# Optimization experiments

Measured on AMD Instinct MI355X. Metric: run time of the kernel, lower is better.

Reference implementation:

```python
import jax, jax.numpy as jnp
import numpy as np

DIM = 512
BATCH = 256
LOG_2PI = float(np.log(2.0 * np.pi))


def setup_inputs() -> dict:
    key = jax.random.key(0)
    k_x, k_mu, k_ld, k_lt, k_m = jax.random.split(key, 5)
    n_tril = DIM * (DIM - 1) // 2  # 130816
    x = jax.random.normal(k_x, (BATCH, DIM), dtype=jnp.float32)
    mu = jax.random.normal(k_mu, (DIM,), dtype=jnp.float32)
    log_diagonal = jax.random.normal(k_ld, (DIM,), dtype=jnp.float32)
    # scale strict-lower entries for reasonable conditioning of cov = A A^T
    lower_tri = jax.random.normal(k_lt, (n_tril,), dtype=jnp.float32) * 0.05
    mask = jax.random.randint(k_m, (BATCH, DIM), 0, 2) > 0
    return {"x": x, "mu": mu, "log_diagonal": log_diagonal,
            "lower_tri": lower_tri, "mask": mask}


def _build_cov(log_diagonal, lower_tri):
    D = log_diagonal.shape[0]
    ti, tj = np.tril_indices(D, -1)
    A = jnp.zeros((D, D), dtype=log_diagonal.dtype).at[ti, tj].set(lower_tri)
    A = A + jnp.diag(jnp.exp(log_diagonal))
    return A @ A.T  # SPD covariance [D, D]


def reference(x, mu, log_diagonal, lower_tri, mask):
    cov = _build_cov(log_diagonal, lower_tri)          # [D, D]
    m = mask.astype(x.dtype)                           # [B, D]
    D = cov.shape[0]
    # Block-diagonalized masked covariance: observed block = cov[m][:,m],
    # unobserved block = identity. Equivalent to per-sample submatrix gather.
    cov_m = (m[:, :, None] * m[:, None, :]) * cov[None] \
            + jnp.eye(D, dtype=x.dtype)[None] * (1.0 - m)[:, :, None]  # [B, D, D]
    L = jnp.linalg.cholesky(cov_m)                     # batched [B, D, D]
    r = (x - mu) * m                                   # masked residual [B, D]
    z = jax.scipy.linalg.solve_triangular(L, r[..., None], lower=True)[..., 0]
    quad = jnp.sum(z * z, axis=-1)                     # [B]
    # unobserved diag of L is 1 -> contributes 0 to logdet
    logdet = 2.0 * jnp.sum(jnp.log(jnp.diagonal(L, axis1=-2, axis2=-1)), axis=-1)
    d_obs = jnp.sum(m, axis=-1)
    return 0.5 * (quad + logdet + d_obs * LOG_2PI)     # neg log prob, [B]
```

## Files before the change

kernel.cpp:

```cpp
#include <hip/hip_runtime.h>
#include <hip/hip_bf16.h>

#define LOG_2PI 1.8378770664093453f
#define R0 256
#define GSTRIDE 512
#define TRI_FLOATS 33280
#define CSTR 68
#define NT 256
#define SMEM_FLOATS (TRI_FLOATS + 512 + 512 + 512 + 16 + 64*CSTR)
#define SMEM_BYTES (SMEM_FLOATS * 4)

__device__ __forceinline__ int tribase(int r) {
    int m = r & 3;
    return r * (r + 1) / 2 + 6 * (r >> 2) + ((m * (7 - m)) >> 1);
}

__global__ __launch_bounds__(256) void build_A(const float* __restrict__ logd,
                                               const float* __restrict__ lt,
                                               float* __restrict__ A) {
    int idx = blockIdx.x * 256 + threadIdx.x;
    int i = idx >> 9, j = idx & 511;
    float v;
    if (j < i)       v = lt[(i * (i - 1)) / 2 + j];
    else if (j == i) v = expf(logd[i]);
    else             v = 0.f;
    A[idx] = v;
}

__global__ __launch_bounds__(256) void aat(const float* __restrict__ A,
                                           float* __restrict__ C) {
    __shared__ float Ash[32][33];
    __shared__ float Bsh[32][33];
    int tx = threadIdx.x & 31, ty = threadIdx.x >> 5;
    int bi = blockIdx.y, bj = blockIdx.x;
    float acc[4] = {0.f, 0.f, 0.f, 0.f};
    for (int k0 = 0; k0 < 512; k0 += 32) {
        #pragma unroll
        for (int q = 0; q < 4; q++) {
            int r = ty + q * 8;
            Ash[r][tx] = A[(bi * 32 + r) * 512 + k0 + tx];
            Bsh[r][tx] = A[(bj * 32 + r) * 512 + k0 + tx];
        }
        __syncthreads();
        for (int c = 0; c < 32; c++) {
            float bv = Bsh[tx][c];
            #pragma unroll
            for (int q = 0; q < 4; q++) acc[q] += Ash[ty + q * 8][c] * bv;
        }
        __syncthreads();
    }
    #pragma unroll
    for (int q = 0; q < 4; q++)
        C[(bi * 32 + ty + q * 8) * 512 + bj * 32 + tx] = acc[q];
}

__global__ __launch_bounds__(256) void compact(const float* __restrict__ x,
                                               const float* __restrict__ mu,
                                               const int* __restrict__ mask,
                                               int* __restrict__ obs_idx,
                                               int* __restrict__ n_obs,
                                               float* __restrict__ rc) {
    int b = blockIdx.x, t = threadIdx.x;
    __shared__ int wsum[4];
    int i0 = 2 * t, i1 = 2 * t + 1;
    int m0 = (mask[b * 512 + i0] != 0) ? 1 : 0;
    int m1 = (mask[b * 512 + i1] != 0) ? 1 : 0;
    int local = m0 + m1;
    int v = local;
    int lane = t & 63, wv = t >> 6;
    #pragma unroll
    for (int off = 1; off < 64; off <<= 1) {
        int u = __shfl_up(v, off, 64);
        if (lane >= off) v += u;
    }
    if (lane == 63) wsum[wv] = v;
    __syncthreads();
    int woff = 0;
    for (int w = 0; w < wv; w++) woff += wsum[w];
    int excl = woff + v - local;
    if (m0) { obs_idx[b * 512 + excl] = i0; rc[b * 512 + excl] = x[b * 512 + i0] - mu[i0]; }
    if (m1) { int p = excl + m0; obs_idx[b * 512 + p] = i1; rc[b * 512 + p] = x[b * 512 + i1] - mu[i1]; }
    if (t == 0) n_obs[b] = wsum[0] + wsum[1] + wsum[2] + wsum[3];
}

template <typename RPF>
__device__ __forceinline__ void diag_block(RPF rptr, float* zsh, float* dinvAll,
                                           float& llog, int j0, int nb, int n, int tid) {
    if (tid < 32) {
        int l = tid;
        int r = j0 + l;
        float a[32];
        float z = 0.f;
        if (r < n) {
            const float4* src = (const float4*)(rptr(r) + j0);
            #pragma unroll
            for (int q = 0; q < 8; q++) {
                float4 t = src[q];
                a[4*q+0] = t.x; a[4*q+1] = t.y; a[4*q+2] = t.z; a[4*q+3] = t.w;
            }
            z = zsh[r];
        } else {
            #pragma unroll
            for (int q = 0; q < 32; q++) a[q] = 0.f;
        }
        float dv = 0.f;
        #pragma unroll
        for (int k = 0; k < 32; k++) {
            if (k < nb) {
                float akk = __shfl(a[k], k, 64);
                float rin = rsqrtf(akk);
                float lkk = akk * rin;
                if (l == k) { dv = rin; llog += __logf(lkk); }
                a[k] = (l == k) ? lkk : a[k] * rin;
                #pragma unroll
                for (int j = k + 1; j < 32; j++) {
                    float ajk = __shfl(a[k], j, 64);
                    a[j] -= a[k] * ajk;
                }
            }
        }
        #pragma unroll
        for (int k = 0; k < 32; k++) {
            if (k < nb) {
                if (l == k) z *= dv;
                float zk = __shfl(z, k, 64);
                if (l > k) z -= a[k] * zk;
            }
        }
        dinvAll[j0 + l] = dv;
        if (l < nb) {
            zsh[r] = z;
            float* dst = rptr(r) + j0;
            #pragma unroll
            for (int c = 0; c < 32; c++)
                if (c <= l) dst[c] = a[c];
        }
    }
}

__global__ __launch_bounds__(NT) void chol_solve(
    const float* __restrict__ cov, const float* __restrict__ rc,
    const int* __restrict__ obs_idx, const int* __restrict__ n_obs,
    float* __restrict__ gtail_all, float* __restrict__ out) {

    extern __shared__ float smem[];
    float* T       = smem;
    float* zsh     = T + TRI_FLOATS;
    int*   oi      = (int*)(zsh + 512);
    float* dinvAll = (float*)(oi + 512);
    float* red     = dinvAll + 512;
    float* SBc     = red + 16;

    int b = blockIdx.x, tid = threadIdx.x;
    int lane = tid & 63, wv = tid >> 6;
    int n = n_obs[b]; if (n > 512) n = 512;
    float* gtail = gtail_all + (size_t)b * 256 * GSTRIDE;
    if (n == 0) { if (tid == 0) out[b] = 0.f; return; }

    for (int i = tid; i < n; i += NT) {
        oi[i] = obs_idx[b * 512 + i];
        zsh[i] = rc[b * 512 + i];
    }
    __syncthreads();

    int n0 = (n < R0) ? n : R0;
    int ntail = n - n0;

    for (int r = wv; r < n0; r += 4) {
        const float* crow = cov + (size_t)oi[r] * 512;
        float* dst = T + tribase(r);
        #pragma unroll 4
        for (int j = lane; j <= r; j += 64) dst[j] = crow[oi[j]];
    }
    for (int r = n0 + wv; r < n; r += 4) {
        const float* crow = cov + (size_t)oi[r] * 512;
        float* dst = gtail + (size_t)(r - n0) * GSTRIDE;
        #pragma unroll 4
        for (int j = lane; j < n0; j += 64) dst[j] = crow[oi[j]];
    }
    __syncthreads();

    float llog = 0.f;

    for (int j0 = 0; j0 < n0; j0 += 32) {
        int nb = min(32, n0 - j0);
        diag_block([&](int r) { return T + tribase(r); },
                   zsh, dinvAll, llog, j0, nb, n0, tid);
        __syncthreads();

        int mL = n0 - j0 - 32; if (mL < 0) mL = 0;
        int mtot = mL + ntail;
        if (mtot > 0) {
            for (int idx = tid; idx < mtot; idx += NT) {
                int r; float* prow;
                if (idx < mL) { r = j0 + 32 + idx; prow = T + tribase(r) + j0; }
                else          { r = n0 + (idx - mL);
                                prow = gtail + (size_t)(idx - mL) * GSTRIDE + j0; }
                float p[32];
                #pragma unroll
                for (int q = 0; q < 8; q++) {
                    float4 t = *(const float4*)&prow[4 * q];
                    p[4*q+0] = t.x; p[4*q+1] = t.y; p[4*q+2] = t.z; p[4*q+3] = t.w;
                }
                #pragma unroll
                for (int j = 0; j < 32; j++) {
                    float acc = p[j];
                    const float* dj = T + tribase(j0 + j) + j0;
                    int jf = j >> 2;
                    for (int q2 = 0; q2 < jf; q2++) {
                        float4 t = *(const float4*)&dj[q2 * 4];
                        acc -= p[q2*4+0]*t.x + p[q2*4+1]*t.y + p[q2*4+2]*t.z + p[q2*4+3]*t.w;
                    }
                    for (int c = jf * 4; c < j; c++) acc -= p[c] * dj[c];
                    p[j] = acc * dinvAll[j0 + j];
                }
                float zu = 0.f;
                #pragma unroll
                for (int q = 0; q < 8; q++) {
                    *(float4*)&prow[4 * q] = make_float4(p[4*q], p[4*q+1], p[4*q+2], p[4*q+3]);
                    float4 zz = *(const float4*)&zsh[j0 + 4 * q];
                    zu += p[4*q]*zz.x + p[4*q+1]*zz.y + p[4*q+2]*zz.z + p[4*q+3]*zz.w;
                }
                zsh[r] -= zu;
            }
            __syncthreads();

            if (mL > 0) {
                int nMac = (mL + 63) >> 6;
                int ty = tid >> 4, tx = tid & 15;
                for (int MI = 0; MI < nMac; MI++)
                    for (int MJ = 0; MJ <= MI; MJ++) {
                        int rbase = j0 + 32 + MI * 64 + ty * 4;
                        int cbase = j0 + 32 + MJ * 64 + tx * 4;
                        if (MI == MJ && cbase > rbase + 3) continue;
                        int ra[4], rb[4];
                        #pragma unroll
                        for (int a = 0; a < 4; a++) {
                            ra[a] = tribase(min(rbase + a, n0 - 1)) + j0;
                            rb[a] = tribase(min(cbase + a, n0 - 1)) + j0;
                        }
                        float acc[4][4];
                        #pragma unroll
                        for (int a = 0; a < 4; a++)
                            #pragma unroll
                            for (int c = 0; c < 4; c++) acc[a][c] = 0.f;
                        #pragma unroll
                        for (int q = 0; q < 8; q++) {
                            float4 av[4], bv[4];
                            #pragma unroll
                            for (int a = 0; a < 4; a++) av[a] = *(const float4*)&T[ra[a] + 4 * q];
                            #pragma unroll
                            for (int c = 0; c < 4; c++) bv[c] = *(const float4*)&T[rb[c] + 4 * q];
                            #pragma unroll
                            for (int a = 0; a < 4; a++)
                                #pragma unroll
                                for (int c = 0; c < 4; c++)
                                    acc[a][c] += av[a].x*bv[c].x + av[a].y*bv[c].y +
                                                 av[a].z*bv[c].z + av[a].w*bv[c].w;
                        }
                        #pragma unroll
                        for (int a = 0; a < 4; a++) {
                            int r = rbase + a;
                            if (r < n0) {
                                float* trow = T + tribase(r);
                                if (cbase + 3 <= r) {
                                    float4 v = *(const float4*)&trow[cbase];
                                    v.x -= acc[a][0]; v.y -= acc[a][1];
                                    v.z -= acc[a][2]; v.w -= acc[a][3];
                                    *(float4*)&trow[cbase] = v;
                                } else {
                                    #pragma unroll
                                    for (int c = 0; c < 4; c++) {
                                        int cl = cbase + c;
                                        if (cl <= r) trow[cl] -= acc[a][c];
                                    }
                                }
                            }
                        }
                    }
            }

            if (ntail > 0 && mL > 0) {
                int nch = mL >> 2;
                int ntask = ntail * nch;
                for (int t = tid; t < ntask; t += NT) {
                    int row = t / nch, ch = t % nch;
                    float* grow = gtail + (size_t)row * GSTRIDE;
                    float w[32];
                    #pragma unroll
                    for (int q = 0; q < 8; q++) {
                        float4 t4 = *(const float4*)&grow[j0 + 4 * q];
                        w[4*q+0] = t4.x; w[4*q+1] = t4.y; w[4*q+2] = t4.z; w[4*q+3] = t4.w;
                    }
                    int jb = j0 + 32 + ch * 4;
                    float acc4[4];
                    #pragma unroll
                    for (int c = 0; c < 4; c++) {
                        const float* dj = T + tribase(jb + c) + j0;
                        float s = 0.f;
                        #pragma unroll
                        for (int q = 0; q < 8; q++) {
                            float4 t4 = *(const float4*)&dj[4 * q];
                            s += w[4*q+0]*t4.x + w[4*q+1]*t4.y + w[4*q+2]*t4.z + w[4*q+3]*t4.w;
                        }
                        acc4[c] = s;
                    }
                    float4 g4 = *(const float4*)&grow[jb];
                    g4.x -= acc4[0]; g4.y -= acc4[1]; g4.z -= acc4[2]; g4.w -= acc4[3];
                    *(float4*)&grow[jb] = g4;
                }
            }
            __syncthreads();
        }
    }

    for (int gs2 = R0; gs2 < n; gs2 += 64) {
        int t1 = min(64, n - gs2);
        int g1 = gs2 - R0;

        for (int cp = R0; cp < gs2; cp += 32) {
            if (tid < t1) {
                int r = gs2 + tid;
                float* row = gtail + (size_t)(r - R0) * GSTRIDE;
                const float* crow = cov + (size_t)oi[r] * 512;
                float zacc = 0.f;
                for (int j = 0; j < 32; j++) {
                    int jj = cp + j;
                    const float* Lrow = gtail + (size_t)(jj - R0) * GSTRIDE;
                    float acc = crow[oi[jj]];
                    for (int c = 0; c < jj; c++) acc -= row[c] * Lrow[c];
                    float wv2 = acc * dinvAll[jj];
                    row[jj] = wv2;
                    zacc += wv2 * zsh[jj];
                }
                zsh[r] -= zacc;
            }
            __syncthreads();
        }

        {
            int npair = t1 * (t1 + 1) / 2;
            for (int e = tid; e < npair; e += NT) {
                int ti = (int)((sqrtf(8.f * (float)e + 1.f) - 1.f) * 0.5f);
                while ((ti + 1) * (ti + 2) / 2 <= e) ti++;
                while (ti * (ti + 1) / 2 > e) ti--;
                int tj = e - ti * (ti + 1) / 2;
                const float* wa = gtail + (size_t)(g1 + ti) * GSTRIDE;
                const float* wb = gtail + (size_t)(g1 + tj) * GSTRIDE;
                float s = 0.f;
                for (int k = 0; k < gs2; k += 4) {
                    float4 a4 = *(const float4*)&wa[k];
                    float4 b4 = *(const float4*)&wb[k];
                    s += a4.x*b4.x + a4.y*b4.y + a4.z*b4.z + a4.w*b4.w;
                }
                SBc[ti * CSTR + tj] = cov[(size_t)oi[gs2 + ti] * 512 + oi[gs2 + tj]] - s;
            }
        }
        __syncthreads();

        auto crptr = [&](int r) { return SBc + (r - gs2) * CSTR - gs2; };
        diag_block(crptr, zsh, dinvAll, llog, gs2, min(32, t1), n, tid);
        __syncthreads();
        if (t1 > 32) {
            int t2 = t1 - 32;
            if (tid < t2) {
                int r = gs2 + 32 + tid;
                float* prow = SBc + (32 + tid) * CSTR;
                float p[32];
                #pragma unroll
                for (int q = 0; q < 8; q++) {
                    float4 t = *(const float4*)&prow[4 * q];
                    p[4*q+0] = t.x; p[4*q+1] = t.y; p[4*q+2] = t.z; p[4*q+3] = t.w;
                }
                #pragma unroll
                for (int j = 0; j < 32; j++) {
                    float acc = p[j];
                    const float* dj = SBc + j * CSTR;
                    for (int c = 0; c < j; c++) acc -= p[c] * dj[c];
                    p[j] = acc * dinvAll[gs2 + j];
                }
                float zu = 0.f;
                #pragma unroll
                for (int q = 0; q < 8; q++) {
                    *(float4*)&prow[4 * q] = make_float4(p[4*q], p[4*q+1], p[4*q+2], p[4*q+3]);
                    float4 zz = *(const float4*)&zsh[gs2 + 4 * q];
                    zu += p[4*q]*zz.x + p[4*q+1]*zz.y + p[4*q+2]*zz.z + p[4*q+3]*zz.w;
                }
                zsh[r] -= zu;
            }
            __syncthreads();
            int np2 = t2 * (t2 + 1) / 2;
            for (int e = tid; e < np2; e += NT) {
                int ti = (int)((sqrtf(8.f * (float)e + 1.f) - 1.f) * 0.5f);
                while ((ti + 1) * (ti + 2) / 2 <= e) ti++;
                while (ti * (ti + 1) / 2 > e) ti--;
                int tj = e - ti * (ti + 1) / 2;
                const float* wa = SBc + (32 + ti) * CSTR;
                const float* wb = SBc + (32 + tj) * CSTR;
                float s = 0.f;
                #pragma unroll
                for (int q = 0; q < 8; q++) {
                    float4 a4 = *(const float4*)&wa[4 * q];
                    float4 b4 = *(const float4*)&wb[4 * q];
                    s += a4.x*b4.x + a4.y*b4.y + a4.z*b4.z + a4.w*b4.w;
                }
                SBc[(32 + ti) * CSTR + 32 + tj] -= s;
            }
            __syncthreads();
            diag_block(crptr, zsh, dinvAll, llog, gs2 + 32, min(32, t2), n, tid);
            __syncthreads();
        }
        if (gs2 + 64 < n) {
            for (int e = tid; e < t1 * t1; e += NT) {
                int i = e >> 6, j = e & 63;
                if (j <= i && i < t1)
                    gtail[(size_t)(g1 + i) * GSTRIDE + gs2 + j] = SBc[i * CSTR + j];
            }
            __syncthreads();
        }
    }

    float q = 0.f;
    for (int ii = tid; ii < n; ii += NT) { float zv = zsh[ii]; q += zv * zv; }
    #pragma unroll
    for (int off = 32; off; off >>= 1) {
        q    += __shfl_down(q, off, 64);
        llog += __shfl_down(llog, off, 64);
    }
    if (lane == 0) { red[wv] = q; red[8 + wv] = llog; }
    __syncthreads();
    if (tid == 0) {
        float qt = red[0] + red[1] + red[2] + red[3];
        float ls = red[8] + red[9] + red[10] + red[11];
        out[b] = 0.5f * (qt + 2.f * ls + (float)n * LOG_2PI);
    }
}

extern "C" void kernel_launch(void* const* d_in, const int* in_sizes, int n_in,
                              void* d_out, int out_size, void* d_ws, size_t ws_size,
                              hipStream_t stream) {
    const float* x    = (const float*)d_in[0];
    const float* mu   = (const float*)d_in[1];
    const float* logd = (const float*)d_in[2];
    const float* lt   = (const float*)d_in[3];
    const int*   mask = (const int*)d_in[4];
    float* out = (float*)d_out;

    char* ws = (char*)d_ws;
    float* cov     = (float*)(ws);
    float* A       = (float*)(ws + 1048576);
    int*   n_obs   = (int*)  (ws + 2097152);
    int*   obs_idx = (int*)  (ws + 2098176);
    float* rc      = (float*)(ws + 2622464);
    float* gtail   = (float*)(ws + 3146752);

    (void)hipFuncSetAttribute((const void*)chol_solve,
                              hipFuncAttributeMaxDynamicSharedMemorySize,
                              SMEM_BYTES);

    build_A<<<1024, 256, 0, stream>>>(logd, lt, A);
    dim3 g(16, 16);
    aat<<<g, 256, 0, stream>>>(A, cov);
    compact<<<256, 256, 0, stream>>>(x, mu, mask, obs_idx, n_obs, rc);
    chol_solve<<<256, NT, SMEM_BYTES, stream>>>(cov, rc, obs_idx, n_obs, gtail, out);
}
```

Before: 409.4 us.

## Overlap next diagonal-block factorization with trailing update via wave specialization

Restructures the blocked Cholesky loop into a lookahead schedule. Wave 0 updates the next 32-column panel and immediately factors its diagonal block. The other three waves update the remaining trailing submatrix and the global-memory tail rows at the same time. This removes one barrier per block and takes the serial diagonal factorization off the critical path. Several dot products are also split into four independent accumulators with float4 loads to shorten FMA dependency chains, at the cost of more registers and slightly different rounding.

```diff
diff --git a/kernel.cpp b/kernel.cpp
--- a/kernel.cpp
+++ b/kernel.cpp
@@ -138,6 +138,54 @@
     }
 }
 
+__device__ __forceinline__ void syrk_tile4(float* T, int rbase, int cbase,
+                                           int j0, int n0) {
+    int ra[4], rb[4];
+    #pragma unroll
+    for (int a = 0; a < 4; a++) {
+        ra[a] = tribase(min(rbase + a, n0 - 1)) + j0;
+        rb[a] = tribase(min(cbase + a, n0 - 1)) + j0;
+    }
+    float acc[4][4];
+    #pragma unroll
+    for (int a = 0; a < 4; a++)
+        #pragma unroll
+        for (int c = 0; c < 4; c++) acc[a][c] = 0.f;
+    #pragma unroll
+    for (int q = 0; q < 8; q++) {
+        float4 av[4], bv[4];
+        #pragma unroll
+        for (int a = 0; a < 4; a++) av[a] = *(const float4*)&T[ra[a] + 4 * q];
+        #pragma unroll
+        for (int c = 0; c < 4; c++) bv[c] = *(const float4*)&T[rb[c] + 4 * q];
+        #pragma unroll
+        for (int a = 0; a < 4; a++)
+            #pragma unroll
+            for (int c = 0; c < 4; c++)
+                acc[a][c] += av[a].x*bv[c].x + av[a].y*bv[c].y +
+                             av[a].z*bv[c].z + av[a].w*bv[c].w;
+    }
+    #pragma unroll
+    for (int a = 0; a < 4; a++) {
+        int r = rbase + a;
+        if (r < n0) {
+            float* trow = T + tribase(r);
+            if (cbase + 3 <= r) {
+                float4 v = *(const float4*)&trow[cbase];
+                v.x -= acc[a][0]; v.y -= acc[a][1];
+                v.z -= acc[a][2]; v.w -= acc[a][3];
+                *(float4*)&trow[cbase] = v;
+            } else {
+                #pragma unroll
+                for (int c = 0; c < 4; c++) {
+                    int cl = cbase + c;
+                    if (cl <= r) trow[cl] -= acc[a][c];
+                }
+            }
+        }
+    }
+}
+
 __global__ __launch_bounds__(NT) void chol_solve(
     const float* __restrict__ cov, const float* __restrict__ rc,
     const int* __restrict__ obs_idx, const int* __restrict__ n_obs,
@@ -182,108 +230,82 @@
 
     float llog = 0.f;
 
+    diag_block([&](int r) { return T + tribase(r); },
+               zsh, dinvAll, llog, 0, min(32, n0), n0, tid);
+    __syncthreads();
+
     for (int j0 = 0; j0 < n0; j0 += 32) {
-        int nb = min(32, n0 - j0);
-        diag_block([&](int r) { return T + tribase(r); },
-                   zsh, dinvAll, llog, j0, nb, n0, tid);
-        __syncthreads();
-
         int mL = n0 - j0 - 32; if (mL < 0) mL = 0;
         int mtot = mL + ntail;
-        if (mtot > 0) {
-            for (int idx = tid; idx < mtot; idx += NT) {
-                int r; float* prow;
-                if (idx < mL) { r = j0 + 32 + idx; prow = T + tribase(r) + j0; }
-                else          { r = n0 + (idx - mL);
-                                prow = gtail + (size_t)(idx - mL) * GSTRIDE + j0; }
-                float p[32];
-                #pragma unroll
-                for (int q = 0; q < 8; q++) {
-                    float4 t = *(const float4*)&prow[4 * q];
-                    p[4*q+0] = t.x; p[4*q+1] = t.y; p[4*q+2] = t.z; p[4*q+3] = t.w;
-                }
-                #pragma unroll
-                for (int j = 0; j < 32; j++) {
-                    float acc = p[j];
-                    const float* dj = T + tribase(j0 + j) + j0;
-                    int jf = j >> 2;
-                    for (int q2 = 0; q2 < jf; q2++) {
-                        float4 t = *(const float4*)&dj[q2 * 4];
-                        acc -= p[q2*4+0]*t.x + p[q2*4+1]*t.y + p[q2*4+2]*t.z + p[q2*4+3]*t.w;
-                    }
-                    for (int c = jf * 4; c < j; c++) acc -= p[c] * dj[c];
-                    p[j] = acc * dinvAll[j0 + j];
-                }
-                float zu = 0.f;
-                #pragma unroll
-                for (int q = 0; q < 8; q++) {
-                    *(float4*)&prow[4 * q] = make_float4(p[4*q], p[4*q+1], p[4*q+2], p[4*q+3]);
-                    float4 zz = *(const float4*)&zsh[j0 + 4 * q];
-                    zu += p[4*q]*zz.x + p[4*q+1]*zz.y + p[4*q+2]*zz.z + p[4*q+3]*zz.w;
-                }
-                zsh[r] -= zu;
-            }
-            __syncthreads();
-
+        if (mtot == 0) break;
+
+        for (int idx = tid; idx < mtot; idx += NT) {
+            int r; float* prow;
+            if (idx < mL) { r = j0 + 32 + idx; prow = T + tribase(r) + j0; }
+            else          { r = n0 + (idx - mL);
+                            prow = gtail + (size_t)(idx - mL) * GSTRIDE + j0; }
+            float p[32];
+            #pragma unroll
+            for (int q = 0; q < 8; q++) {
+                float4 t = *(const float4*)&prow[4 * q];
+                p[4*q+0] = t.x; p[4*q+1] = t.y; p[4*q+2] = t.z; p[4*q+3] = t.w;
+            }
+            #pragma unroll
+            for (int j = 0; j < 32; j++) {
+                const float* dj = T + tribase(j0 + j) + j0;
+                float s0 = 0.f, s1 = 0.f, s2 = 0.f, s3 = 0.f;
+                int jf = j >> 2;
+                for (int q2 = 0; q2 < jf; q2++) {
+                    float4 t = *(const float4*)&dj[q2 * 4];
+                    s0 += p[q2*4+0]*t.x; s1 += p[q2*4+1]*t.y;
+                    s2 += p[q2*4+2]*t.z; s3 += p[q2*4+3]*t.w;
+                }
+                float acc = p[j] - ((s0 + s1) + (s2 + s3));
+                for (int c = jf * 4; c < j; c++) acc -= p[c] * dj[c];
+                p[j] = acc * dinvAll[j0 + j];
+            }
+            float zu = 0.f;
+            #pragma unroll
+            for (int q = 0; q < 8; q++) {
+                *(float4*)&prow[4 * q] = make_float4(p[4*q], p[4*q+1], p[4*q+2], p[4*q+3]);
+                float4 zz = *(const float4*)&zsh[j0 + 4 * q];
+                zu += p[4*q]*zz.x + p[4*q+1]*zz.y + p[4*q+2]*zz.z + p[4*q+3]*zz.w;
+            }
+            zsh[r] -= zu;
+        }
+        __syncthreads();
+
+        if (wv == 0) {
             if (mL > 0) {
-                int nMac = (mL + 63) >> 6;
-                int ty = tid >> 4, tx = tid & 15;
-                for (int MI = 0; MI < nMac; MI++)
-                    for (int MJ = 0; MJ <= MI; MJ++) {
-                        int rbase = j0 + 32 + MI * 64 + ty * 4;
-                        int cbase = j0 + 32 + MJ * 64 + tx * 4;
-                        if (MI == MJ && cbase > rbase + 3) continue;
-                        int ra[4], rb[4];
-                        #pragma unroll
-                        for (int a = 0; a < 4; a++) {
-                            ra[a] = tribase(min(rbase + a, n0 - 1)) + j0;
-                            rb[a] = tribase(min(cbase + a, n0 - 1)) + j0;
-                        }
-                        float acc[4][4];
-                        #pragma unroll
-                        for (int a = 0; a < 4; a++)
-                            #pragma unroll
-                            for (int c = 0; c < 4; c++) acc[a][c] = 0.f;
-                        #pragma unroll
-                        for (int q = 0; q < 8; q++) {
-                            float4 av[4], bv[4];
-                            #pragma unroll
-                            for (int a = 0; a < 4; a++) av[a] = *(const float4*)&T[ra[a] + 4 * q];
-                            #pragma unroll
-                            for (int c = 0; c < 4; c++) bv[c] = *(const float4*)&T[rb[c] + 4 * q];
-                            #pragma unroll
-                            for (int a = 0; a < 4; a++)
-                                #pragma unroll
-                                for (int c = 0; c < 4; c++)
-                                    acc[a][c] += av[a].x*bv[c].x + av[a].y*bv[c].y +
-                                                 av[a].z*bv[c].z + av[a].w*bv[c].w;
-                        }
-                        #pragma unroll
-                        for (int a = 0; a < 4; a++) {
-                            int r = rbase + a;
-                            if (r < n0) {
-                                float* trow = T + tribase(r);
-                                if (cbase + 3 <= r) {
-                                    float4 v = *(const float4*)&trow[cbase];
-                                    v.x -= acc[a][0]; v.y -= acc[a][1];
-                                    v.z -= acc[a][2]; v.w -= acc[a][3];
-                                    *(float4*)&trow[cbase] = v;
-                                } else {
-                                    #pragma unroll
-                                    for (int c = 0; c < 4; c++) {
-                                        int cl = cbase + c;
-                                        if (cl <= r) trow[cl] -= acc[a][c];
-                                    }
-                                }
-                            }
-                        }
-                    }
-            }
-
+                for (int e = lane; e < 36; e += 64) {
+                    int ti = 0;
+                    while ((ti + 1) * (ti + 2) / 2 <= e) ti++;
+                    int tj = e - ti * (ti + 1) / 2;
+                    syrk_tile4(T, j0 + 32 + ti * 4, j0 + 32 + tj * 4, j0, n0);
+                }
+                __threadfence_block();
+                diag_block([&](int r) { return T + tribase(r); },
+                           zsh, dinvAll, llog, j0 + 32, min(32, mL), n0, tid);
+            }
+        } else {
+            int t7 = tid - 64;
+            int mrest = n0 - j0 - 64;
+            if (mrest > 0) {
+                int rtiles = (mrest + 3) >> 2;
+                int total = rtiles * 9 + rtiles * (rtiles - 1) / 2;
+                for (int e = t7; e < total; e += (NT - 64)) {
+                    int ri = (int)((sqrtf(8.f * (float)e + 289.f) - 17.f) * 0.5f);
+                    if (ri < 0) ri = 0;
+                    while (9 * (ri + 1) + (ri + 1) * ri / 2 <= e) ri++;
+                    while (9 * ri + ri * (ri - 1) / 2 > e) ri--;
+                    int cj = e - (9 * ri + ri * (ri - 1) / 2);
+                    syrk_tile4(T, j0 + 64 + ri * 4, j0 + 32 + cj * 4, j0, n0);
+                }
+            }
             if (ntail > 0 && mL > 0) {
                 int nch = mL >> 2;
                 int ntask = ntail * nch;
-                for (int t = tid; t < ntask; t += NT) {
+                for (int t = t7; t < ntask; t += (NT - 64)) {
                     int row = t / nch, ch = t % nch;
                     float* grow = gtail + (size_t)row * GSTRIDE;
                     float w[32];
@@ -297,21 +319,22 @@
                     #pragma unroll
                     for (int c = 0; c < 4; c++) {
                         const float* dj = T + tribase(jb + c) + j0;
-                        float s = 0.f;
+                        float s0 = 0.f, s1 = 0.f, s2 = 0.f, s3 = 0.f;
                         #pragma unroll
                         for (int q = 0; q < 8; q++) {
                             float4 t4 = *(const float4*)&dj[4 * q];
-                            s += w[4*q+0]*t4.x + w[4*q+1]*t4.y + w[4*q+2]*t4.z + w[4*q+3]*t4.w;
+                            s0 += w[4*q+0]*t4.x; s1 += w[4*q+1]*t4.y;
+                            s2 += w[4*q+2]*t4.z; s3 += w[4*q+3]*t4.w;
                         }
-                        acc4[c] = s;
+                        acc4[c] = (s0 + s1) + (s2 + s3);
                     }
                     float4 g4 = *(const float4*)&grow[jb];
                     g4.x -= acc4[0]; g4.y -= acc4[1]; g4.z -= acc4[2]; g4.w -= acc4[3];
                     *(float4*)&grow[jb] = g4;
                 }
             }
-            __syncthreads();
-        }
+        }
+        __syncthreads();
     }
 
     for (int gs2 = R0; gs2 < n; gs2 += 64) {
@@ -327,8 +350,16 @@
                 for (int j = 0; j < 32; j++) {
                     int jj = cp + j;
                     const float* Lrow = gtail + (size_t)(jj - R0) * GSTRIDE;
-                    float acc = crow[oi[jj]];
-                    for (int c = 0; c < jj; c++) acc -= row[c] * Lrow[c];
+                    float s0 = 0.f, s1 = 0.f, s2 = 0.f, s3 = 0.f;
+                    int jv = jj >> 2;
+                    for (int c4 = 0; c4 < jv; c4++) {
+                        float4 a4 = *(const float4*)&row[c4 * 4];
+                        float4 b4 = *(const float4*)&Lrow[c4 * 4];
+                        s0 += a4.x*b4.x; s1 += a4.y*b4.y;
+                        s2 += a4.z*b4.z; s3 += a4.w*b4.w;
+                    }
+                    float acc = crow[oi[jj]] - ((s0 + s1) + (s2 + s3));
+                    for (int c = jv * 4; c < jj; c++) acc -= row[c] * Lrow[c];
                     float wv2 = acc * dinvAll[jj];
                     row[jj] = wv2;
                     zacc += wv2 * zsh[jj];
@@ -347,13 +378,15 @@
                 int tj = e - ti * (ti + 1) / 2;
                 const float* wa = gtail + (size_t)(g1 + ti) * GSTRIDE;
                 const float* wb = gtail + (size_t)(g1 + tj) * GSTRIDE;
-                float s = 0.f;
+                float s0 = 0.f, s1 = 0.f, s2 = 0.f, s3 = 0.f;
                 for (int k = 0; k < gs2; k += 4) {
                     float4 a4 = *(const float4*)&wa[k];
                     float4 b4 = *(const float4*)&wb[k];
-                    s += a4.x*b4.x + a4.y*b4.y + a4.z*b4.z + a4.w*b4.w;
-                }
-                SBc[ti * CSTR + tj] = cov[(size_t)oi[gs2 + ti] * 512 + oi[gs2 + tj]] - s;
+                    s0 += a4.x*b4.x; s1 += a4.y*b4.y;
+                    s2 += a4.z*b4.z; s3 += a4.w*b4.w;
+                }
+                SBc[ti * CSTR + tj] = cov[(size_t)oi[gs2 + ti] * 512 + oi[gs2 + tj]]
+                                      - ((s0 + s1) + (s2 + s3));
             }
         }
         __syncthreads();
@@ -374,9 +407,16 @@
                 }
                 #pragma unroll
                 for (int j = 0; j < 32; j++) {
-                    float acc = p[j];
                     const float* dj = SBc + j * CSTR;
-                    for (int c = 0; c < j; c++) acc -= p[c] * dj[c];
+                    float s0 = 0.f, s1 = 0.f, s2 = 0.f, s3 = 0.f;
+                    int jf = j >> 2;
+                    for (int q2 = 0; q2 < jf; q2++) {
+                        float4 t = *(const float4*)&dj[q2 * 4];
+                        s0 += p[q2*4+0]*t.x; s1 += p[q2*4+1]*t.y;
+                        s2 += p[q2*4+2]*t.z; s3 += p[q2*4+3]*t.w;
+                    }
+                    float acc = p[j] - ((s0 + s1) + (s2 + s3));
+                    for (int c = jf * 4; c < j; c++) acc -= p[c] * dj[c];
                     p[j] = acc * dinvAll[gs2 + j];
                 }
                 float zu = 0.f;
@@ -397,14 +437,15 @@
                 int tj = e - ti * (ti + 1) / 2;
                 const float* wa = SBc + (32 + ti) * CSTR;
                 const float* wb = SBc + (32 + tj) * CSTR;
-                float s = 0.f;
+                float s0 = 0.f, s1 = 0.f, s2 = 0.f, s3 = 0.f;
                 #pragma unroll
                 for (int q = 0; q < 8; q++) {
                     float4 a4 = *(const float4*)&wa[4 * q];
                     float4 b4 = *(const float4*)&wb[4 * q];
-                    s += a4.x*b4.x + a4.y*b4.y + a4.z*b4.z + a4.w*b4.w;
-                }
-                SBc[(32 + ti) * CSTR + 32 + tj] -= s;
+                    s0 += a4.x*b4.x; s1 += a4.y*b4.y;
+                    s2 += a4.z*b4.z; s3 += a4.w*b4.w;
+                }
+                SBc[(32 + ti) * CSTR + 32 + tj] -= (s0 + s1) + (s2 + s3);
             }
             __syncthreads();
             diag_block(crptr, zsh, dinvAll, llog, gs2 + 32, min(32, t2), n, tid);
```

After: 517.6 us. +26.4%, slower.
